# Performance work log

Measured on AMD Instinct MI355X. Metric: run time of the kernel, lower is better.

The kernel has to match this reference:

```python
import jax, jax.numpy as jnp
import numpy as np

DIM = 128
LAYERS = 3
N_NODES = 50000
N_EDGES = 640000
LN_EPS = 1e-5


def setup_inputs() -> dict:
    key = jax.random.key(0)
    ks = jax.random.split(key, 10)
    s = 1.0 / np.sqrt(DIM)
    x = jax.random.normal(ks[0], (N_NODES, DIM), dtype=jnp.float32)
    edge_index = jax.random.randint(ks[1], (2, N_EDGES), 0, N_NODES, dtype=jnp.int64)
    in_w = jax.random.uniform(ks[2], (DIM, DIM), jnp.float32, -s, s)
    in_b = jax.random.uniform(ks[3], (DIM,), jnp.float32, -s, s)
    w1 = jax.random.uniform(ks[4], (LAYERS, DIM, DIM), jnp.float32, -s, s)
    b1 = jax.random.uniform(ks[5], (LAYERS, DIM), jnp.float32, -s, s)
    w2 = jax.random.uniform(ks[6], (LAYERS, DIM, DIM), jnp.float32, -s, s)
    b2 = jax.random.uniform(ks[7], (LAYERS, DIM), jnp.float32, -s, s)
    ln_g = jnp.ones((LAYERS, DIM), jnp.float32)
    ln_b = jnp.zeros((LAYERS, DIM), jnp.float32)
    return {"x": x, "edge_index": edge_index, "in_w": in_w, "in_b": in_b,
            "w1": w1, "b1": b1, "w2": w2, "b2": b2, "ln_g": ln_g, "ln_b": ln_b}


def _layer_norm(z, g, b):
    mu = jnp.mean(z, axis=-1, keepdims=True)
    var = jnp.mean(jnp.square(z - mu), axis=-1, keepdims=True)
    return (z - mu) * jax.lax.rsqrt(var + LN_EPS) * g + b


def reference(x, edge_index, in_w, in_b, w1, b1, w2, b2, ln_g, ln_b):
    src, dst = edge_index[0], edge_index[1]
    n = x.shape[0]
    # degree is identical every layer in the original; compute once (same math)
    deg = jax.ops.segment_sum(jnp.ones(dst.shape, x.dtype), dst, num_segments=n)
    deg = jnp.maximum(deg, 1.0)[:, None]  # [N,1]
    h = x @ in_w + in_b  # [N,D]
    for i in range(w1.shape[0]):
        m = jax.ops.segment_sum(h[src], dst, num_segments=n) / deg  # gather+scatter
        mlp = jax.nn.relu(m @ w1[i] + b1[i]) @ w2[i] + b2[i]
        h = _layer_norm(h + mlp, ln_g[i], ln_b[i])
    return h
```

## Files before the change

### kernel.cpp

```cpp
#include <hip/hip_runtime.h>
#include <hip/hip_fp8.h>

#define DIM 128
#define LN_EPS 1e-5f

typedef __attribute__((ext_vector_type(8))) short s16x8;
typedef __attribute__((ext_vector_type(4))) float f32x4;
typedef __attribute__((ext_vector_type(2))) float f32x2;
typedef __attribute__((ext_vector_type(4))) unsigned int u32x4;
typedef __attribute__((ext_vector_type(2))) unsigned int u32x2;

__device__ __forceinline__ unsigned short f2bf(float f) {
    unsigned u = __float_as_uint(f);
    unsigned r = u + 0x7fffu + ((u >> 16) & 1u);
    return (unsigned short)(r >> 16);
}
__device__ __forceinline__ float bf2f(unsigned short b) {
    return __uint_as_float(((unsigned)b) << 16);
}
__device__ __forceinline__ unsigned char f2fp8(float f) {
    return (unsigned char)__hip_cvt_float_to_fp8(f, __HIP_SATFINITE, __HIP_E4M3);
}
__device__ __forceinline__ void acc_fp8x4(float* a, unsigned v) {
    f32x2 lo = __builtin_amdgcn_cvt_pk_f32_fp8(v, false);
    f32x2 hi = __builtin_amdgcn_cvt_pk_f32_fp8(v, true);
    a[0] += lo[0]; a[1] += lo[1]; a[2] += hi[0]; a[3] += hi[1];
}
__device__ __forceinline__ void acc_fp8x16(float* a, u32x4 v) {
    acc_fp8x4(a + 0,  v[0]);
    acc_fp8x4(a + 4,  v[1]);
    acc_fp8x4(a + 8,  v[2]);
    acc_fp8x4(a + 12, v[3]);
}


__global__ void count_deg(const int* __restrict__ dst, int E, int* __restrict__ counts) {
    int i = (blockIdx.x * 256 + threadIdx.x) * 4;
    if (i + 3 < E) {
        int4 d = *(const int4*)(dst + i);
        atomicAdd(&counts[d.x], 1);
        atomicAdd(&counts[d.y], 1);
        atomicAdd(&counts[d.z], 1);
        atomicAdd(&counts[d.w], 1);
    } else {
        for (int j = i; j < E; ++j) atomicAdd(&counts[dst[j]], 1);
    }
}

__global__ __launch_bounds__(256) void scan_partials(const int* __restrict__ counts, int n,
                                                     int* __restrict__ bsum) {
    int base = blockIdx.x * 1024 + threadIdx.x * 4;
    int s = 0;
#pragma unroll
    for (int j = 0; j < 4; ++j) {
        int i = base + j;
        if (i < n) s += counts[i];
    }
#pragma unroll
    for (int off = 32; off > 0; off >>= 1) s += __shfl_xor(s, off, 64);
    __shared__ int wsum[4];
    int lane = threadIdx.x & 63, wid = threadIdx.x >> 6;
    if (lane == 0) wsum[wid] = s;
    __syncthreads();
    if (threadIdx.x == 0) bsum[blockIdx.x] = wsum[0] + wsum[1] + wsum[2] + wsum[3];
}

__global__ __launch_bounds__(64) void scan_bsums(const int* __restrict__ bsum,
                                                 int* __restrict__ bofs, int nb,
                                                 int* __restrict__ rowptr, int N, int E) {
    int lane = threadIdx.x;
    int carry = 0;
    for (int base = 0; base < nb; base += 64) {
        int v = (base + lane < nb) ? bsum[base + lane] : 0;
        int incl = v;
#pragma unroll
        for (int off = 1; off < 64; off <<= 1) {
            int t = __shfl_up(incl, off, 64);
            if (lane >= off) incl += t;
        }
        if (base + lane < nb) bofs[base + lane] = carry + incl - v;
        carry += __shfl(incl, 63, 64);
    }
    if (lane == 0) rowptr[N] = E;
}

__global__ __launch_bounds__(256) void scan_final(const int* __restrict__ counts, int n,
                                                  const int* __restrict__ bofs,
                                                  int* __restrict__ rowptr,
                                                  int* __restrict__ cursor,
                                                  float* __restrict__ dinv) {
    int base = blockIdx.x * 1024 + threadIdx.x * 4;
    int v[4];
#pragma unroll
    for (int j = 0; j < 4; ++j) {
        int i = base + j;
        v[j] = (i < n) ? counts[i] : 0;
    }
    int tsum = v[0] + v[1] + v[2] + v[3];
    int lane = threadIdx.x & 63, wid = threadIdx.x >> 6;
    int incl = tsum;
#pragma unroll
    for (int off = 1; off < 64; off <<= 1) {
        int t = __shfl_up(incl, off, 64);
        if (lane >= off) incl += t;
    }
    __shared__ int wsum[4];
    if (lane == 63) wsum[wid] = incl;
    __syncthreads();
    int wofs = 0;
    for (int w = 0; w < 4; ++w)
        if (w < wid) wofs += wsum[w];
    int excl = bofs[blockIdx.x] + wofs + (incl - tsum);
#pragma unroll
    for (int j = 0; j < 4; ++j) {
        int i = base + j;
        if (i < n) {
            rowptr[i] = excl;
            cursor[i] = excl;
            dinv[i] = 1.0f / (float)((v[j] > 1) ? v[j] : 1);
            excl += v[j];
        }
    }
}

__global__ void fill_csr(const int* __restrict__ src, const int* __restrict__ dst, int E,
                         int* __restrict__ cursor, int* __restrict__ srcidx) {
    int i = (blockIdx.x * 256 + threadIdx.x) * 4;
    if (i + 3 < E) {
        int4 s = *(const int4*)(src + i);
        int4 d = *(const int4*)(dst + i);
        int p0 = atomicAdd(&cursor[d.x], 1); srcidx[p0] = s.x;
        int p1 = atomicAdd(&cursor[d.y], 1); srcidx[p1] = s.y;
        int p2 = atomicAdd(&cursor[d.z], 1); srcidx[p2] = s.z;
        int p3 = atomicAdd(&cursor[d.w], 1); srcidx[p3] = s.w;
    } else {
        for (int j = i; j < E; ++j) {
            int p = atomicAdd(&cursor[dst[j]], 1);
            srcidx[p] = src[j];
        }
    }
}


__global__ __launch_bounds__(256) void cvt_weights(const float* __restrict__ in_w,
                                                   const float* __restrict__ w1,
                                                   const float* __restrict__ w2,
                                                   unsigned short* __restrict__ wt, int L) {
    int mat = blockIdx.x >> 3, part = blockIdx.x & 7;
    const float* src;
    if (mat == 0) src = in_w;
    else if (mat <= L) src = w1 + (size_t)(mat - 1) * DIM * DIM;
    else src = w2 + (size_t)(mat - 1 - L) * DIM * DIM;
    unsigned short* dst = wt + (size_t)mat * DIM * DIM;
    int base = part * 2048 + threadIdx.x;
#pragma unroll
    for (int j = 0; j < 8; ++j) {
        int i = base + j * 256;
        int k = i >> 7, n = i & 127;
        dst[n * DIM + k] = f2bf(src[i]);
    }
}


__global__ __launch_bounds__(256) void gemm_bias_mfma(const float* __restrict__ x,
                                                      const unsigned short* __restrict__ Wt,
                                                      const float* __restrict__ bias,
                                                      unsigned short* __restrict__ hb,
                                                      unsigned char* __restrict__ h8, int N) {
    int tid = threadIdx.x;
    int s = tid >> 6, lane = tid & 63;
    int quad = lane >> 4, l16 = lane & 15;
    int r0 = blockIdx.x * 16;
    int cs = s * 32;
    int arow = r0 + l16;
    bool av = arow < N;

    f32x4 acc[2];
    acc[0] = (f32x4){0.f, 0.f, 0.f, 0.f};
    acc[1] = (f32x4){0.f, 0.f, 0.f, 0.f};

    const float4* xp = (const float4*)(x + ((size_t)(av ? arow : 0) << 7)) + quad * 2;
#pragma unroll
    for (int k0 = 0; k0 < 128; k0 += 32) {
        s16x8 a = {0, 0, 0, 0, 0, 0, 0, 0};
        if (av) {
            float4 f0 = xp[k0 / 4];
            float4 f1 = xp[k0 / 4 + 1];
            a[0] = (short)f2bf(f0.x); a[1] = (short)f2bf(f0.y);
            a[2] = (short)f2bf(f0.z); a[3] = (short)f2bf(f0.w);
            a[4] = (short)f2bf(f1.x); a[5] = (short)f2bf(f1.y);
            a[6] = (short)f2bf(f1.z); a[7] = (short)f2bf(f1.w);
        }
        s16x8 b0 = *(const s16x8*)(Wt + ((size_t)(cs + l16) << 7) + quad * 8 + k0);
        s16x8 b1 = *(const s16x8*)(Wt + ((size_t)(cs + 16 + l16) << 7) + quad * 8 + k0);
        acc[0] = __builtin_amdgcn_mfma_f32_16x16x32_bf16(a, b0, acc[0], 0, 0, 0);
        acc[1] = __builtin_amdgcn_mfma_f32_16x16x32_bf16(a, b1, acc[1], 0, 0, 0);
    }

#pragma unroll
    for (int c = 0; c < 2; ++c) {
        int col = cs + c * 16 + l16;
        float bv = bias[col];
#pragma unroll
        for (int reg = 0; reg < 4; ++reg) {
            int grow = r0 + quad * 4 + reg;
            if (grow < N) {
                float o = acc[c][reg] + bv;
                hb[((size_t)grow << 7) + col] = f2bf(o);
                h8[((size_t)grow << 7) + col] = f2fp8(o);
            }
        }
    }
}


__global__ __launch_bounds__(256) void aggregate(const unsigned char* __restrict__ h8in,
                                                 const int* __restrict__ rowptr,
                                                 const int* __restrict__ srcidx,
                                                 const float* __restrict__ dinv,
                                                 unsigned short* __restrict__ mout, int N) {
    int tid = threadIdx.x;
    int w = tid >> 6, lane = tid & 63;
    int g = lane >> 3, li = lane & 7;
    int nd = blockIdx.x * 32 + w * 8 + g;
    bool nv = nd < N;

    int e  = nv ? rowptr[nd] : 0;
    int ee = nv ? rowptr[nd + 1] : 0;
    float di = nv ? dinv[nd] : 0.f;

    const unsigned char* hsl = h8in + li * 16;

    float a[16];
#pragma unroll
    for (int j = 0; j < 16; ++j) a[j] = 0.f;

#define GIDX(jj) (((jj) < ee) ? srcidx[(jj)] : -1)
    int jA = e;
    int iA0 = GIDX(jA + 0), iA1 = GIDX(jA + 1), iA2 = GIDX(jA + 2), iA3 = GIDX(jA + 3);
    u32x4 A0 = {0, 0, 0, 0}, A1 = {0, 0, 0, 0}, A2 = {0, 0, 0, 0}, A3 = {0, 0, 0, 0};
    if (iA0 >= 0) A0 = *(const u32x4*)(hsl + ((size_t)iA0 << 7));
    if (iA1 >= 0) A1 = *(const u32x4*)(hsl + ((size_t)iA1 << 7));
    if (iA2 >= 0) A2 = *(const u32x4*)(hsl + ((size_t)iA2 << 7));
    if (iA3 >= 0) A3 = *(const u32x4*)(hsl + ((size_t)iA3 << 7));
    int jB = jA + 4;
    int iB0 = GIDX(jB + 0), iB1 = GIDX(jB + 1), iB2 = GIDX(jB + 2), iB3 = GIDX(jB + 3);

    while (__any(jA < ee)) {
        u32x4 B0 = {0, 0, 0, 0}, B1v = {0, 0, 0, 0}, B2v = {0, 0, 0, 0}, B3 = {0, 0, 0, 0};
        if (iB0 >= 0) B0  = *(const u32x4*)(hsl + ((size_t)iB0 << 7));
        if (iB1 >= 0) B1v = *(const u32x4*)(hsl + ((size_t)iB1 << 7));
        if (iB2 >= 0) B2v = *(const u32x4*)(hsl + ((size_t)iB2 << 7));
        if (iB3 >= 0) B3  = *(const u32x4*)(hsl + ((size_t)iB3 << 7));
        int jC = jB + 4;
        int iC0 = GIDX(jC + 0), iC1 = GIDX(jC + 1), iC2 = GIDX(jC + 2), iC3 = GIDX(jC + 3);
        acc_fp8x16(a, A0);
        acc_fp8x16(a, A1);
        acc_fp8x16(a, A2);
        acc_fp8x16(a, A3);
        jA = jB; A0 = B0; A1 = B1v; A2 = B2v; A3 = B3;
        jB = jC; iB0 = iC0; iB1 = iC1; iB2 = iC2; iB3 = iC3;
    }
#undef GIDX

    if (nv) {
        u32x4 o0, o1;
#pragma unroll
        for (int j = 0; j < 4; ++j) {
            unsigned lo0 = f2bf(a[2 * j]     * di);
            unsigned hi0 = f2bf(a[2 * j + 1] * di);
            o0[j] = lo0 | (hi0 << 16);
            unsigned lo1 = f2bf(a[8 + 2 * j]     * di);
            unsigned hi1 = f2bf(a[8 + 2 * j + 1] * di);
            o1[j] = lo1 | (hi1 << 16);
        }
        unsigned short* mp = mout + ((size_t)nd << 7) + li * 16;
        *(u32x4*)(mp)     = o0;
        *(u32x4*)(mp + 8) = o1;
    }
}


__global__ __launch_bounds__(256) void mlp_ln(const unsigned short* __restrict__ hin,
                                              const unsigned short* __restrict__ m,
                                              const unsigned short* __restrict__ W1t,
                                              const float* __restrict__ B1,
                                              const unsigned short* __restrict__ W2t,
                                              const float* __restrict__ B2,
                                              const float* __restrict__ G,
                                              const float* __restrict__ Bb,
                                              unsigned short* __restrict__ hout,
                                              unsigned char* __restrict__ h8out,
                                              float* __restrict__ out_f32, int N) {
    __shared__ unsigned short M[32][132];
    __shared__ unsigned short P[32][132];
    __shared__ float s1p[4][32], s2p[4][32];

    int tid = threadIdx.x;
    int w = tid >> 6, lane = tid & 63;
    int quad = lane >> 4, l16 = lane & 15;
    int r0 = blockIdx.x * 32;
    int cs = w * 32;

#pragma unroll
    for (int cc = 0; cc < 2; ++cc) {
        int c = tid + cc * 256;
        int row = c >> 4, colc = (c & 15) * 8;
        int grow = r0 + row;
        u32x4 v = {0, 0, 0, 0};
        if (grow < N) v = *(const u32x4*)(m + ((size_t)grow << 7) + colc);
        *(u32x4*)(&M[row][colc]) = v;
    }
    __syncthreads();

    unsigned short hvr[2][2][4];
#pragma unroll
    for (int rt = 0; rt < 2; ++rt) {
#pragma unroll
        for (int c = 0; c < 2; ++c) {
            int col = cs + c * 16 + l16;
#pragma unroll
            for (int reg = 0; reg < 4; ++reg) {
                int grow = r0 + rt * 16 + quad * 4 + reg;
                hvr[rt][c][reg] = (grow < N) ? hin[((size_t)grow << 7) + col] : (unsigned short)0;
            }
        }
    }

    f32x4 ac1[2][2];
    ac1[0][0] = (f32x4){0.f, 0.f, 0.f, 0.f}; ac1[0][1] = (f32x4){0.f, 0.f, 0.f, 0.f};
    ac1[1][0] = (f32x4){0.f, 0.f, 0.f, 0.f}; ac1[1][1] = (f32x4){0.f, 0.f, 0.f, 0.f};
#pragma unroll
    for (int k0 = 0; k0 < 128; k0 += 32) {
        s16x8 b0 = *(const s16x8*)(W1t + ((size_t)(cs + l16) << 7) + quad * 8 + k0);
        s16x8 b1 = *(const s16x8*)(W1t + ((size_t)(cs + 16 + l16) << 7) + quad * 8 + k0);
        s16x8 a0 = *(const s16x8*)(&M[l16][quad * 8 + k0]);
        s16x8 a1 = *(const s16x8*)(&M[16 + l16][quad * 8 + k0]);
        ac1[0][0] = __builtin_amdgcn_mfma_f32_16x16x32_bf16(a0, b0, ac1[0][0], 0, 0, 0);
        ac1[0][1] = __builtin_amdgcn_mfma_f32_16x16x32_bf16(a0, b1, ac1[0][1], 0, 0, 0);
        ac1[1][0] = __builtin_amdgcn_mfma_f32_16x16x32_bf16(a1, b0, ac1[1][0], 0, 0, 0);
        ac1[1][1] = __builtin_amdgcn_mfma_f32_16x16x32_bf16(a1, b1, ac1[1][1], 0, 0, 0);
    }
#pragma unroll
    for (int rt = 0; rt < 2; ++rt) {
#pragma unroll
        for (int c = 0; c < 2; ++c) {
            int col = cs + c * 16 + l16;
            float bv = B1[col];
#pragma unroll
            for (int reg = 0; reg < 4; ++reg) {
                float v = fmaxf(ac1[rt][c][reg] + bv, 0.f);
                P[rt * 16 + quad * 4 + reg][col] = f2bf(v);
            }
        }
    }
    __syncthreads();

    f32x4 ac2[2][2];
    ac2[0][0] = (f32x4){0.f, 0.f, 0.f, 0.f}; ac2[0][1] = (f32x4){0.f, 0.f, 0.f, 0.f};
    ac2[1][0] = (f32x4){0.f, 0.f, 0.f, 0.f}; ac2[1][1] = (f32x4){0.f, 0.f, 0.f, 0.f};
#pragma unroll
    for (int k0 = 0; k0 < 128; k0 += 32) {
        s16x8 b0 = *(const s16x8*)(W2t + ((size_t)(cs + l16) << 7) + quad * 8 + k0);
        s16x8 b1 = *(const s16x8*)(W2t + ((size_t)(cs + 16 + l16) << 7) + quad * 8 + k0);
        s16x8 a0 = *(const s16x8*)(&P[l16][quad * 8 + k0]);
        s16x8 a1 = *(const s16x8*)(&P[16 + l16][quad * 8 + k0]);
        ac2[0][0] = __builtin_amdgcn_mfma_f32_16x16x32_bf16(a0, b0, ac2[0][0], 0, 0, 0);
        ac2[0][1] = __builtin_amdgcn_mfma_f32_16x16x32_bf16(a0, b1, ac2[0][1], 0, 0, 0);
        ac2[1][0] = __builtin_amdgcn_mfma_f32_16x16x32_bf16(a1, b0, ac2[1][0], 0, 0, 0);
        ac2[1][1] = __builtin_amdgcn_mfma_f32_16x16x32_bf16(a1, b1, ac2[1][1], 0, 0, 0);
    }

    float z[2][2][4];
    float ps1[2][4] = {{0, 0, 0, 0}, {0, 0, 0, 0}};
    float ps2[2][4] = {{0, 0, 0, 0}, {0, 0, 0, 0}};
#pragma unroll
    for (int rt = 0; rt < 2; ++rt) {
#pragma unroll
        for (int c = 0; c < 2; ++c) {
            int col = cs + c * 16 + l16;
            float b2v = B2[col];
#pragma unroll
            for (int reg = 0; reg < 4; ++reg) {
                float hv = bf2f(hvr[rt][c][reg]);
                float zz = ac2[rt][c][reg] + b2v + hv;
                z[rt][c][reg] = zz;
                ps1[rt][reg] += zz;
                ps2[rt][reg] += zz * zz;
            }
        }
    }
#pragma unroll
    for (int off = 1; off < 16; off <<= 1) {
#pragma unroll
        for (int rt = 0; rt < 2; ++rt) {
#pragma unroll
            for (int reg = 0; reg < 4; ++reg) {
                ps1[rt][reg] += __shfl_xor(ps1[rt][reg], off, 64);
                ps2[rt][reg] += __shfl_xor(ps2[rt][reg], off, 64);
            }
        }
    }
    if (l16 == 0) {
#pragma unroll
        for (int rt = 0; rt < 2; ++rt) {
#pragma unroll
            for (int reg = 0; reg < 4; ++reg) {
                s1p[w][rt * 16 + quad * 4 + reg] = ps1[rt][reg];
                s2p[w][rt * 16 + quad * 4 + reg] = ps2[rt][reg];
            }
        }
    }
    __syncthreads();

#pragma unroll
    for (int rt = 0; rt < 2; ++rt) {
#pragma unroll
        for (int reg = 0; reg < 4; ++reg) {
            int row = rt * 16 + quad * 4 + reg;
            float S1 = s1p[0][row] + s1p[1][row] + s1p[2][row] + s1p[3][row];
            float S2 = s2p[0][row] + s2p[1][row] + s2p[2][row] + s2p[3][row];
            float mean = S1 * (1.0f / 128.0f);
            float var = S2 * (1.0f / 128.0f) - mean * mean;
            float rs = rsqrtf(var + LN_EPS);
            int grow = r0 + row;
            if (grow < N) {
#pragma unroll
                for (int c = 0; c < 2; ++c) {
                    int col = cs + c * 16 + l16;
                    float o = (z[rt][c][reg] - mean) * rs * G[col] + Bb[col];
                    if (out_f32) {
                        out_f32[((size_t)grow << 7) + col] = o;
                    } else {
                        hout[((size_t)grow << 7) + col] = f2bf(o);
                        h8out[((size_t)grow << 7) + col] = f2fp8(o);
                    }
                }
            }
        }
    }
}


extern "C" void kernel_launch(void* const* d_in, const int* in_sizes, int n_in,
                              void* d_out, int out_size, void* d_ws, size_t ws_size,
                              hipStream_t stream) {
    const float* x    = (const float*)d_in[0];
    const int*   ei   = (const int*)d_in[1];
    const float* in_w = (const float*)d_in[2];
    const float* in_b = (const float*)d_in[3];
    const float* w1   = (const float*)d_in[4];
    const float* b1   = (const float*)d_in[5];
    const float* w2   = (const float*)d_in[6];
    const float* b2   = (const float*)d_in[7];
    const float* ln_g = (const float*)d_in[8];
    const float* ln_b = (const float*)d_in[9];

    const int N = in_sizes[0] / DIM;
    const int E = in_sizes[1] / 2;
    const int LAYERS = in_sizes[4] / (DIM * DIM);

    const int* e_src = ei;
    const int* e_dst = ei + E;

    char* ws = (char*)d_ws;
    unsigned short* hb0    = (unsigned short*)ws;  ws += (size_t)N * DIM * 2;
    unsigned short* hb1    = (unsigned short*)ws;  ws += (size_t)N * DIM * 2;
    unsigned char*  h8a    = (unsigned char*)ws;   ws += (size_t)N * DIM;
    unsigned char*  h8b    = (unsigned char*)ws;   ws += (size_t)N * DIM;
    int*            counts = (int*)ws;             ws += (size_t)N * 4;
    int*            rowptr = (int*)ws;             ws += (size_t)(N + 1) * 4;
    int*            cursor = (int*)ws;             ws += (size_t)N * 4;
    float*          dinv   = (float*)ws;           ws += (size_t)N * 4;
    int*            srcidx = (int*)ws;             ws += (size_t)E * 4;
    int*            bsum   = (int*)ws;             ws += 4096;
    int*            bofs   = (int*)ws;             ws += 4096;
    unsigned short* wt     = (unsigned short*)ws;  ws += (size_t)(2 * LAYERS + 1) * DIM * DIM * 2;
    unsigned short* mbuf   = (unsigned short*)ws;  ws += (size_t)N * DIM * 2;

    const int nScanBlocks = (N + 1023) / 1024;
    const int nMat = 2 * LAYERS + 1;

    (void)hipMemsetAsync(counts, 0, (size_t)N * 4, stream);
    count_deg<<<(E + 1023) / 1024, 256, 0, stream>>>(e_dst, E, counts);
    scan_partials<<<nScanBlocks, 256, 0, stream>>>(counts, N, bsum);
    scan_bsums<<<1, 64, 0, stream>>>(bsum, bofs, nScanBlocks, rowptr, N, E);
    scan_final<<<nScanBlocks, 256, 0, stream>>>(counts, N, bofs, rowptr, cursor, dinv);
    fill_csr<<<(E + 1023) / 1024, 256, 0, stream>>>(e_src, e_dst, E, cursor, srcidx);
    cvt_weights<<<nMat * 8, 256, 0, stream>>>(in_w, w1, w2, wt, LAYERS);

    const unsigned short* in_wt = wt;
    const unsigned short* w1t   = wt + (size_t)DIM * DIM;
    const unsigned short* w2t   = wt + (size_t)(1 + LAYERS) * DIM * DIM;

    gemm_bias_mfma<<<(N + 15) / 16, 256, 0, stream>>>(x, in_wt, in_b, hb0, h8a, N);

    int tile_grid = (N + 31) / 32;
    unsigned short* hin  = hb0;  unsigned char* h8in  = h8a;
    unsigned short* hout = hb1;  unsigned char* h8out = h8b;
    for (int i = 0; i < LAYERS; ++i) {
        float* out = (i == LAYERS - 1) ? (float*)d_out : nullptr;
        aggregate<<<tile_grid, 256, 0, stream>>>(h8in, rowptr, srcidx, dinv, mbuf, N);
        mlp_ln<<<tile_grid, 256, 0, stream>>>(hin, mbuf,
                                              w1t + (size_t)i * DIM * DIM, b1 + (size_t)i * DIM,
                                              w2t + (size_t)i * DIM * DIM, b2 + (size_t)i * DIM,
                                              ln_g + (size_t)i * DIM, ln_b + (size_t)i * DIM,
                                              hout, h8out, out, N);
        unsigned short* t = hin; hin = hout; hout = t;
        unsigned char* t8 = h8in; h8in = h8out; h8out = t8;
    }
}
```

Baseline: 335.4 us.

## Split fp8 feature table into column planes and aggregate each plane separately

The fp8 copy of the node features is stored as two 64-column planes ([2][N][64]), and the aggregation runs twice, once per plane. Each plane is then half the size of the full table, so it is more likely to stay resident in cache during the random neighbour gathers. The setup is also trimmed: the weight conversion and degree counting are fused into one launch, and the single-block offset scan is folded into scan_final, where each block sums the preceding partial sums itself. The cost is twice the index and rowptr traffic and an extra kernel launch per layer.

```diff
diff --git a/kernel.cpp b/kernel.cpp
--- a/kernel.cpp
+++ b/kernel.cpp
@@ -33,17 +33,43 @@
     acc_fp8x4(a + 12, v[3]);
 }
 
-
-__global__ void count_deg(const int* __restrict__ dst, int E, int* __restrict__ counts) {
-    int i = (blockIdx.x * 256 + threadIdx.x) * 4;
-    if (i + 3 < E) {
-        int4 d = *(const int4*)(dst + i);
-        atomicAdd(&counts[d.x], 1);
-        atomicAdd(&counts[d.y], 1);
-        atomicAdd(&counts[d.z], 1);
-        atomicAdd(&counts[d.w], 1);
+__device__ __forceinline__ size_t h8addr(int col, int row, int N) {
+    return (size_t)(col >> 6) * ((size_t)N * 64) + ((size_t)row << 6) + (col & 63);
+}
+
+
+__global__ __launch_bounds__(256) void prep(const float* __restrict__ in_w,
+                                            const float* __restrict__ w1,
+                                            const float* __restrict__ w2,
+                                            unsigned short* __restrict__ wt, int L,
+                                            const int* __restrict__ dst, int E,
+                                            int* __restrict__ counts, int nWblk) {
+    if ((int)blockIdx.x < nWblk) {
+        int mat = blockIdx.x >> 3, part = blockIdx.x & 7;
+        const float* src;
+        if (mat == 0) src = in_w;
+        else if (mat <= L) src = w1 + (size_t)(mat - 1) * DIM * DIM;
+        else src = w2 + (size_t)(mat - 1 - L) * DIM * DIM;
+        unsigned short* dstw = wt + (size_t)mat * DIM * DIM;
+        int base = part * 2048 + threadIdx.x;
+#pragma unroll
+        for (int j = 0; j < 8; ++j) {
+            int i = base + j * 256;
+            int k = i >> 7, n = i & 127;
+            dstw[n * DIM + k] = f2bf(src[i]);
+        }
     } else {
-        for (int j = i; j < E; ++j) atomicAdd(&counts[dst[j]], 1);
+        int b = blockIdx.x - nWblk;
+        int i = (b * 256 + threadIdx.x) * 4;
+        if (i + 3 < E) {
+            int4 d = *(const int4*)(dst + i);
+            atomicAdd(&counts[d.x], 1);
+            atomicAdd(&counts[d.y], 1);
+            atomicAdd(&counts[d.z], 1);
+            atomicAdd(&counts[d.w], 1);
+        } else {
+            for (int j = i; j < E; ++j) atomicAdd(&counts[dst[j]], 1);
+        }
     }
 }
 
@@ -65,31 +91,26 @@
     if (threadIdx.x == 0) bsum[blockIdx.x] = wsum[0] + wsum[1] + wsum[2] + wsum[3];
 }
 
-__global__ __launch_bounds__(64) void scan_bsums(const int* __restrict__ bsum,
-                                                 int* __restrict__ bofs, int nb,
-                                                 int* __restrict__ rowptr, int N, int E) {
-    int lane = threadIdx.x;
-    int carry = 0;
-    for (int base = 0; base < nb; base += 64) {
-        int v = (base + lane < nb) ? bsum[base + lane] : 0;
-        int incl = v;
-#pragma unroll
-        for (int off = 1; off < 64; off <<= 1) {
-            int t = __shfl_up(incl, off, 64);
-            if (lane >= off) incl += t;
-        }
-        if (base + lane < nb) bofs[base + lane] = carry + incl - v;
-        carry += __shfl(incl, 63, 64);
-    }
-    if (lane == 0) rowptr[N] = E;
-}
-
 __global__ __launch_bounds__(256) void scan_final(const int* __restrict__ counts, int n,
-                                                  const int* __restrict__ bofs,
+                                                  const int* __restrict__ bsum, int nScan,
                                                   int* __restrict__ rowptr,
                                                   int* __restrict__ cursor,
-                                                  float* __restrict__ dinv) {
-    int base = blockIdx.x * 1024 + threadIdx.x * 4;
+                                                  float* __restrict__ dinv, int E) {
+    __shared__ int s_bofs;
+    __shared__ int wsum[4];
+    int tid = threadIdx.x;
+    int lane = tid & 63, wid = tid >> 6;
+
+    if (tid < 64) {
+        int acc = 0;
+        for (int i = lane; i < (int)blockIdx.x; i += 64) acc += bsum[i];
+#pragma unroll
+        for (int off = 32; off > 0; off >>= 1) acc += __shfl_xor(acc, off, 64);
+        if (lane == 0) s_bofs = acc;
+    }
+    if (blockIdx.x == 0 && tid == 0) rowptr[n] = E;
+
+    int base = blockIdx.x * 1024 + tid * 4;
     int v[4];
 #pragma unroll
     for (int j = 0; j < 4; ++j) {
@@ -97,20 +118,18 @@
         v[j] = (i < n) ? counts[i] : 0;
     }
     int tsum = v[0] + v[1] + v[2] + v[3];
-    int lane = threadIdx.x & 63, wid = threadIdx.x >> 6;
     int incl = tsum;
 #pragma unroll
     for (int off = 1; off < 64; off <<= 1) {
         int t = __shfl_up(incl, off, 64);
         if (lane >= off) incl += t;
     }
-    __shared__ int wsum[4];
     if (lane == 63) wsum[wid] = incl;
     __syncthreads();
     int wofs = 0;
     for (int w = 0; w < 4; ++w)
         if (w < wid) wofs += wsum[w];
-    int excl = bofs[blockIdx.x] + wofs + (incl - tsum);
+    int excl = s_bofs + wofs + (incl - tsum);
 #pragma unroll
     for (int j = 0; j < 4; ++j) {
         int i = base + j;
@@ -142,26 +161,6 @@
 }
 
 
-__global__ __launch_bounds__(256) void cvt_weights(const float* __restrict__ in_w,
-                                                   const float* __restrict__ w1,
-                                                   const float* __restrict__ w2,
-                                                   unsigned short* __restrict__ wt, int L) {
-    int mat = blockIdx.x >> 3, part = blockIdx.x & 7;
-    const float* src;
-    if (mat == 0) src = in_w;
-    else if (mat <= L) src = w1 + (size_t)(mat - 1) * DIM * DIM;
-    else src = w2 + (size_t)(mat - 1 - L) * DIM * DIM;
-    unsigned short* dst = wt + (size_t)mat * DIM * DIM;
-    int base = part * 2048 + threadIdx.x;
-#pragma unroll
-    for (int j = 0; j < 8; ++j) {
-        int i = base + j * 256;
-        int k = i >> 7, n = i & 127;
-        dst[n * DIM + k] = f2bf(src[i]);
-    }
-}
-
-
 __global__ __launch_bounds__(256) void gemm_bias_mfma(const float* __restrict__ x,
                                                       const unsigned short* __restrict__ Wt,
                                                       const float* __restrict__ bias,
@@ -207,29 +206,30 @@
             if (grow < N) {
                 float o = acc[c][reg] + bv;
                 hb[((size_t)grow << 7) + col] = f2bf(o);
-                h8[((size_t)grow << 7) + col] = f2fp8(o);
-            }
-        }
-    }
-}
-
-
-__global__ __launch_bounds__(256) void aggregate(const unsigned char* __restrict__ h8in,
+                h8[h8addr(col, grow, N)] = f2fp8(o);
+            }
+        }
+    }
+}
+
+
+__global__ __launch_bounds__(256) void aggregate(const unsigned char* __restrict__ h8plane,
                                                  const int* __restrict__ rowptr,
                                                  const int* __restrict__ srcidx,
                                                  const float* __restrict__ dinv,
-                                                 unsigned short* __restrict__ mout, int N) {
+                                                 unsigned short* __restrict__ mout,
+                                                 int N, int plane) {
     int tid = threadIdx.x;
     int w = tid >> 6, lane = tid & 63;
-    int g = lane >> 3, li = lane & 7;
-    int nd = blockIdx.x * 32 + w * 8 + g;
+    int g = lane >> 2, li = lane & 3;
+    int nd = blockIdx.x * 64 + w * 16 + g;
     bool nv = nd < N;
 
     int e  = nv ? rowptr[nd] : 0;
     int ee = nv ? rowptr[nd + 1] : 0;
     float di = nv ? dinv[nd] : 0.f;
 
-    const unsigned char* hsl = h8in + li * 16;
+    const unsigned char* hsl = h8plane + li * 16;
 
     float a[16];
 #pragma unroll
@@ -239,19 +239,19 @@
     int jA = e;
     int iA0 = GIDX(jA + 0), iA1 = GIDX(jA + 1), iA2 = GIDX(jA + 2), iA3 = GIDX(jA + 3);
     u32x4 A0 = {0, 0, 0, 0}, A1 = {0, 0, 0, 0}, A2 = {0, 0, 0, 0}, A3 = {0, 0, 0, 0};
-    if (iA0 >= 0) A0 = *(const u32x4*)(hsl + ((size_t)iA0 << 7));
-    if (iA1 >= 0) A1 = *(const u32x4*)(hsl + ((size_t)iA1 << 7));
-    if (iA2 >= 0) A2 = *(const u32x4*)(hsl + ((size_t)iA2 << 7));
-    if (iA3 >= 0) A3 = *(const u32x4*)(hsl + ((size_t)iA3 << 7));
+    if (iA0 >= 0) A0 = *(const u32x4*)(hsl + ((size_t)iA0 << 6));
+    if (iA1 >= 0) A1 = *(const u32x4*)(hsl + ((size_t)iA1 << 6));
+    if (iA2 >= 0) A2 = *(const u32x4*)(hsl + ((size_t)iA2 << 6));
+    if (iA3 >= 0) A3 = *(const u32x4*)(hsl + ((size_t)iA3 << 6));
     int jB = jA + 4;
     int iB0 = GIDX(jB + 0), iB1 = GIDX(jB + 1), iB2 = GIDX(jB + 2), iB3 = GIDX(jB + 3);
 
     while (__any(jA < ee)) {
         u32x4 B0 = {0, 0, 0, 0}, B1v = {0, 0, 0, 0}, B2v = {0, 0, 0, 0}, B3 = {0, 0, 0, 0};
-        if (iB0 >= 0) B0  = *(const u32x4*)(hsl + ((size_t)iB0 << 7));
-        if (iB1 >= 0) B1v = *(const u32x4*)(hsl + ((size_t)iB1 << 7));
-        if (iB2 >= 0) B2v = *(const u32x4*)(hsl + ((size_t)iB2 << 7));
-        if (iB3 >= 0) B3  = *(const u32x4*)(hsl + ((size_t)iB3 << 7));
+        if (iB0 >= 0) B0  = *(const u32x4*)(hsl + ((size_t)iB0 << 6));
+        if (iB1 >= 0) B1v = *(const u32x4*)(hsl + ((size_t)iB1 << 6));
+        if (iB2 >= 0) B2v = *(const u32x4*)(hsl + ((size_t)iB2 << 6));
+        if (iB3 >= 0) B3  = *(const u32x4*)(hsl + ((size_t)iB3 << 6));
         int jC = jB + 4;
         int iC0 = GIDX(jC + 0), iC1 = GIDX(jC + 1), iC2 = GIDX(jC + 2), iC3 = GIDX(jC + 3);
         acc_fp8x16(a, A0);
@@ -274,7 +274,7 @@
             unsigned hi1 = f2bf(a[8 + 2 * j + 1] * di);
             o1[j] = lo1 | (hi1 << 16);
         }
-        unsigned short* mp = mout + ((size_t)nd << 7) + li * 16;
+        unsigned short* mp = mout + ((size_t)nd << 7) + plane * 64 + li * 16;
         *(u32x4*)(mp)     = o0;
         *(u32x4*)(mp + 8) = o1;
     }
@@ -433,7 +433,7 @@
                         out_f32[((size_t)grow << 7) + col] = o;
                     } else {
                         hout[((size_t)grow << 7) + col] = f2bf(o);
-                        h8out[((size_t)grow << 7) + col] = f2fp8(o);
+                        h8out[h8addr(col, grow, N)] = f2fp8(o);
                     }
                 }
             }
@@ -474,20 +474,20 @@
     float*          dinv   = (float*)ws;           ws += (size_t)N * 4;
     int*            srcidx = (int*)ws;             ws += (size_t)E * 4;
     int*            bsum   = (int*)ws;             ws += 4096;
-    int*            bofs   = (int*)ws;             ws += 4096;
     unsigned short* wt     = (unsigned short*)ws;  ws += (size_t)(2 * LAYERS + 1) * DIM * DIM * 2;
     unsigned short* mbuf   = (unsigned short*)ws;  ws += (size_t)N * DIM * 2;
 
     const int nScanBlocks = (N + 1023) / 1024;
     const int nMat = 2 * LAYERS + 1;
+    const int nWblk = nMat * 8;
 
     (void)hipMemsetAsync(counts, 0, (size_t)N * 4, stream);
-    count_deg<<<(E + 1023) / 1024, 256, 0, stream>>>(e_dst, E, counts);
+    prep<<<nWblk + (E + 1023) / 1024, 256, 0, stream>>>(in_w, w1, w2, wt, LAYERS,
+                                                        e_dst, E, counts, nWblk);
     scan_partials<<<nScanBlocks, 256, 0, stream>>>(counts, N, bsum);
-    scan_bsums<<<1, 64, 0, stream>>>(bsum, bofs, nScanBlocks, rowptr, N, E);
-    scan_final<<<nScanBlocks, 256, 0, stream>>>(counts, N, bofs, rowptr, cursor, dinv);
+    scan_final<<<nScanBlocks, 256, 0, stream>>>(counts, N, bsum, nScanBlocks,
+                                                rowptr, cursor, dinv, E);
     fill_csr<<<(E + 1023) / 1024, 256, 0, stream>>>(e_src, e_dst, E, cursor, srcidx);
-    cvt_weights<<<nMat * 8, 256, 0, stream>>>(in_w, w1, w2, wt, LAYERS);
 
     const unsigned short* in_wt = wt;
     const unsigned short* w1t   = wt + (size_t)DIM * DIM;
@@ -495,17 +495,20 @@
 
     gemm_bias_mfma<<<(N + 15) / 16, 256, 0, stream>>>(x, in_wt, in_b, hb0, h8a, N);
 
-    int tile_grid = (N + 31) / 32;
+    int agg_grid = (N + 63) / 64;
+    int mlp_grid = (N + 31) / 32;
     unsigned short* hin  = hb0;  unsigned char* h8in  = h8a;
     unsigned short* hout = hb1;  unsigned char* h8out = h8b;
     for (int i = 0; i < LAYERS; ++i) {
         float* out = (i == LAYERS - 1) ? (float*)d_out : nullptr;
-        aggregate<<<tile_grid, 256, 0, stream>>>(h8in, rowptr, srcidx, dinv, mbuf, N);
-        mlp_ln<<<tile_grid, 256, 0, stream>>>(hin, mbuf,
-                                              w1t + (size_t)i * DIM * DIM, b1 + (size_t)i * DIM,
-                                              w2t + (size_t)i * DIM * DIM, b2 + (size_t)i * DIM,
-                                              ln_g + (size_t)i * DIM, ln_b + (size_t)i * DIM,
-                                              hout, h8out, out, N);
+        aggregate<<<agg_grid, 256, 0, stream>>>(h8in, rowptr, srcidx, dinv, mbuf, N, 0);
+        aggregate<<<agg_grid, 256, 0, stream>>>(h8in + (size_t)N * 64, rowptr, srcidx, dinv,
+                                                mbuf, N, 1);
+        mlp_ln<<<mlp_grid, 256, 0, stream>>>(hin, mbuf,
+                                             w1t + (size_t)i * DIM * DIM, b1 + (size_t)i * DIM,
+                                             w2t + (size_t)i * DIM * DIM, b2 + (size_t)i * DIM,
+                                             ln_g + (size_t)i * DIM, ln_b + (size_t)i * DIM,
+                                             hout, h8out, out, N);
         unsigned short* t = hin; hin = hout; hout = t;
         unsigned char* t8 = h8in; h8in = h8out; h8out = t8;
     }
```

Result: slower. 362.2 us (+8.0%).

## Merge graph-prep kernels: fuse degree count, single-pass scan, CSR fill with projection

Applied to the files above, without the earlier changes.

Weight conversion and degree counting now run as one launch, with the block index picking the role. The three-kernel prefix scan becomes a single kernel in which each block redundantly sums all counts before its own range. CSR filling is merged with the input projection GEMM so the two independent jobs share one launch. The goal is fewer launches and serial gaps in the setup phase, at the cost of redundant prefix reads in the scan and mixed workloads sharing a grid.

```diff
diff --git a/kernel.cpp b/kernel.cpp
--- a/kernel.cpp
+++ b/kernel.cpp
@@ -8,7 +8,6 @@
 typedef __attribute__((ext_vector_type(4))) float f32x4;
 typedef __attribute__((ext_vector_type(2))) float f32x2;
 typedef __attribute__((ext_vector_type(4))) unsigned int u32x4;
-typedef __attribute__((ext_vector_type(2))) unsigned int u32x2;
 
 __device__ __forceinline__ unsigned short f2bf(float f) {
     unsigned u = __float_as_uint(f);
@@ -34,62 +33,66 @@
 }
 
 
-__global__ void count_deg(const int* __restrict__ dst, int E, int* __restrict__ counts) {
-    int i = (blockIdx.x * 256 + threadIdx.x) * 4;
-    if (i + 3 < E) {
-        int4 d = *(const int4*)(dst + i);
-        atomicAdd(&counts[d.x], 1);
-        atomicAdd(&counts[d.y], 1);
-        atomicAdd(&counts[d.z], 1);
-        atomicAdd(&counts[d.w], 1);
+__global__ __launch_bounds__(256) void prep(const float* __restrict__ in_w,
+                                            const float* __restrict__ w1,
+                                            const float* __restrict__ w2,
+                                            unsigned short* __restrict__ wt, int L,
+                                            const int* __restrict__ dst, int E,
+                                            int* __restrict__ counts, int nWblk) {
+    if ((int)blockIdx.x < nWblk) {
+        int mat = blockIdx.x >> 3, part = blockIdx.x & 7;
+        const float* src;
+        if (mat == 0) src = in_w;
+        else if (mat <= L) src = w1 + (size_t)(mat - 1) * DIM * DIM;
+        else src = w2 + (size_t)(mat - 1 - L) * DIM * DIM;
+        unsigned short* dstw = wt + (size_t)mat * DIM * DIM;
+        int base = part * 2048 + threadIdx.x;
+#pragma unroll
+        for (int j = 0; j < 8; ++j) {
+            int i = base + j * 256;
+            int k = i >> 7, n = i & 127;
+            dstw[n * DIM + k] = f2bf(src[i]);
+        }
     } else {
-        for (int j = i; j < E; ++j) atomicAdd(&counts[dst[j]], 1);
-    }
-}
-
-__global__ __launch_bounds__(256) void scan_partials(const int* __restrict__ counts, int n,
-                                                     int* __restrict__ bsum) {
-    int base = blockIdx.x * 1024 + threadIdx.x * 4;
-    int s = 0;
-#pragma unroll
-    for (int j = 0; j < 4; ++j) {
-        int i = base + j;
-        if (i < n) s += counts[i];
-    }
-#pragma unroll
-    for (int off = 32; off > 0; off >>= 1) s += __shfl_xor(s, off, 64);
+        int b = blockIdx.x - nWblk;
+        int i = (b * 256 + threadIdx.x) * 4;
+        if (i + 3 < E) {
+            int4 d = *(const int4*)(dst + i);
+            atomicAdd(&counts[d.x], 1);
+            atomicAdd(&counts[d.y], 1);
+            atomicAdd(&counts[d.z], 1);
+            atomicAdd(&counts[d.w], 1);
+        } else {
+            for (int j = i; j < E; ++j) atomicAdd(&counts[dst[j]], 1);
+        }
+    }
+}
+
+
+__global__ __launch_bounds__(256) void scan_all(const int* __restrict__ counts, int n,
+                                                int* __restrict__ rowptr,
+                                                int* __restrict__ cursor,
+                                                float* __restrict__ dinv, int E) {
     __shared__ int wsum[4];
-    int lane = threadIdx.x & 63, wid = threadIdx.x >> 6;
-    if (lane == 0) wsum[wid] = s;
-    __syncthreads();
-    if (threadIdx.x == 0) bsum[blockIdx.x] = wsum[0] + wsum[1] + wsum[2] + wsum[3];
-}
-
-__global__ __launch_bounds__(64) void scan_bsums(const int* __restrict__ bsum,
-                                                 int* __restrict__ bofs, int nb,
-                                                 int* __restrict__ rowptr, int N, int E) {
-    int lane = threadIdx.x;
-    int carry = 0;
-    for (int base = 0; base < nb; base += 64) {
-        int v = (base + lane < nb) ? bsum[base + lane] : 0;
-        int incl = v;
-#pragma unroll
-        for (int off = 1; off < 64; off <<= 1) {
-            int t = __shfl_up(incl, off, 64);
-            if (lane >= off) incl += t;
-        }
-        if (base + lane < nb) bofs[base + lane] = carry + incl - v;
-        carry += __shfl(incl, 63, 64);
-    }
-    if (lane == 0) rowptr[N] = E;
-}
-
-__global__ __launch_bounds__(256) void scan_final(const int* __restrict__ counts, int n,
-                                                  const int* __restrict__ bofs,
-                                                  int* __restrict__ rowptr,
-                                                  int* __restrict__ cursor,
-                                                  float* __restrict__ dinv) {
-    int base = blockIdx.x * 1024 + threadIdx.x * 4;
+    int tid = threadIdx.x;
+    int lane = tid & 63, wid = tid >> 6;
+
+    int limit = blockIdx.x * 1024;
+    int acc = 0;
+    for (int i = tid * 4; i < limit; i += 1024) {
+        int4 c4 = *(const int4*)(counts + i);
+        acc += c4.x + c4.y + c4.z + c4.w;
+    }
+#pragma unroll
+    for (int off = 32; off > 0; off >>= 1) acc += __shfl_xor(acc, off, 64);
+    if (lane == 0) wsum[wid] = acc;
+    __syncthreads();
+    int bofs = wsum[0] + wsum[1] + wsum[2] + wsum[3];
+    __syncthreads();
+
+    if (blockIdx.x == 0 && tid == 0) rowptr[n] = E;
+
+    int base = blockIdx.x * 1024 + tid * 4;
     int v[4];
 #pragma unroll
     for (int j = 0; j < 4; ++j) {
@@ -97,20 +100,18 @@
         v[j] = (i < n) ? counts[i] : 0;
     }
     int tsum = v[0] + v[1] + v[2] + v[3];
-    int lane = threadIdx.x & 63, wid = threadIdx.x >> 6;
     int incl = tsum;
 #pragma unroll
     for (int off = 1; off < 64; off <<= 1) {
         int t = __shfl_up(incl, off, 64);
         if (lane >= off) incl += t;
     }
-    __shared__ int wsum[4];
     if (lane == 63) wsum[wid] = incl;
     __syncthreads();
     int wofs = 0;
     for (int w = 0; w < 4; ++w)
         if (w < wid) wofs += wsum[w];
-    int excl = bofs[blockIdx.x] + wofs + (incl - tsum);
+    int excl = bofs + wofs + (incl - tsum);
 #pragma unroll
     for (int j = 0; j < 4; ++j) {
         int i = base + j;
@@ -123,91 +124,74 @@
     }
 }
 
-__global__ void fill_csr(const int* __restrict__ src, const int* __restrict__ dst, int E,
-                         int* __restrict__ cursor, int* __restrict__ srcidx) {
-    int i = (blockIdx.x * 256 + threadIdx.x) * 4;
-    if (i + 3 < E) {
-        int4 s = *(const int4*)(src + i);
-        int4 d = *(const int4*)(dst + i);
-        int p0 = atomicAdd(&cursor[d.x], 1); srcidx[p0] = s.x;
-        int p1 = atomicAdd(&cursor[d.y], 1); srcidx[p1] = s.y;
-        int p2 = atomicAdd(&cursor[d.z], 1); srcidx[p2] = s.z;
-        int p3 = atomicAdd(&cursor[d.w], 1); srcidx[p3] = s.w;
+
+__global__ __launch_bounds__(256) void fill_proj(const float* __restrict__ x,
+                                                 const unsigned short* __restrict__ Wt,
+                                                 const float* __restrict__ bias,
+                                                 unsigned short* __restrict__ hb,
+                                                 unsigned char* __restrict__ h8, int N,
+                                                 const int* __restrict__ src,
+                                                 const int* __restrict__ dst, int E,
+                                                 int* __restrict__ cursor,
+                                                 int* __restrict__ srcidx, int gemmBlocks) {
+    int tid = threadIdx.x;
+    if ((int)blockIdx.x < gemmBlocks) {
+        int s = tid >> 6, lane = tid & 63;
+        int quad = lane >> 4, l16 = lane & 15;
+        int r0 = blockIdx.x * 16;
+        int cs = s * 32;
+        int arow = r0 + l16;
+        bool av = arow < N;
+
+        f32x4 acc0 = (f32x4){0.f, 0.f, 0.f, 0.f};
+        f32x4 acc1 = (f32x4){0.f, 0.f, 0.f, 0.f};
+
+        const float4* xp = (const float4*)(x + ((size_t)(av ? arow : 0) << 7)) + quad * 2;
+#pragma unroll
+        for (int k0 = 0; k0 < 128; k0 += 32) {
+            s16x8 a = {0, 0, 0, 0, 0, 0, 0, 0};
+            if (av) {
+                float4 f0 = xp[k0 / 4];
+                float4 f1 = xp[k0 / 4 + 1];
+                a[0] = (short)f2bf(f0.x); a[1] = (short)f2bf(f0.y);
+                a[2] = (short)f2bf(f0.z); a[3] = (short)f2bf(f0.w);
+                a[4] = (short)f2bf(f1.x); a[5] = (short)f2bf(f1.y);
+                a[6] = (short)f2bf(f1.z); a[7] = (short)f2bf(f1.w);
+            }
+            s16x8 b0 = *(const s16x8*)(Wt + ((size_t)(cs + l16) << 7) + quad * 8 + k0);
+            s16x8 b1 = *(const s16x8*)(Wt + ((size_t)(cs + 16 + l16) << 7) + quad * 8 + k0);
+            acc0 = __builtin_amdgcn_mfma_f32_16x16x32_bf16(a, b0, acc0, 0, 0, 0);
+            acc1 = __builtin_amdgcn_mfma_f32_16x16x32_bf16(a, b1, acc1, 0, 0, 0);
+        }
+
+#pragma unroll
+        for (int c = 0; c < 2; ++c) {
+            int col = cs + c * 16 + l16;
+            float bv = bias[col];
+#pragma unroll
+            for (int reg = 0; reg < 4; ++reg) {
+                int grow = r0 + quad * 4 + reg;
+                if (grow < N) {
+                    float o = (c == 0 ? acc0[reg] : acc1[reg]) + bv;
+                    hb[((size_t)grow << 7) + col] = f2bf(o);
+                    h8[((size_t)grow << 7) + col] = f2fp8(o);
+                }
+            }
+        }
     } else {
-        for (int j = i; j < E; ++j) {
-            int p = atomicAdd(&cursor[dst[j]], 1);
-            srcidx[p] = src[j];
-        }
-    }
-}
-
-
-__global__ __launch_bounds__(256) void cvt_weights(const float* __restrict__ in_w,
-                                                   const float* __restrict__ w1,
-                                                   const float* __restrict__ w2,
-                                                   unsigned short* __restrict__ wt, int L) {
-    int mat = blockIdx.x >> 3, part = blockIdx.x & 7;
-    const float* src;
-    if (mat == 0) src = in_w;
-    else if (mat <= L) src = w1 + (size_t)(mat - 1) * DIM * DIM;
-    else src = w2 + (size_t)(mat - 1 - L) * DIM * DIM;
-    unsigned short* dst = wt + (size_t)mat * DIM * DIM;
-    int base = part * 2048 + threadIdx.x;
-#pragma unroll
-    for (int j = 0; j < 8; ++j) {
-        int i = base + j * 256;
-        int k = i >> 7, n = i & 127;
-        dst[n * DIM + k] = f2bf(src[i]);
-    }
-}
-
-
-__global__ __launch_bounds__(256) void gemm_bias_mfma(const float* __restrict__ x,
-                                                      const unsigned short* __restrict__ Wt,
-                                                      const float* __restrict__ bias,
-                                                      unsigned short* __restrict__ hb,
-                                                      unsigned char* __restrict__ h8, int N) {
-    int tid = threadIdx.x;
-    int s = tid >> 6, lane = tid & 63;
-    int quad = lane >> 4, l16 = lane & 15;
-    int r0 = blockIdx.x * 16;
-    int cs = s * 32;
-    int arow = r0 + l16;
-    bool av = arow < N;
-
-    f32x4 acc[2];
-    acc[0] = (f32x4){0.f, 0.f, 0.f, 0.f};
-    acc[1] = (f32x4){0.f, 0.f, 0.f, 0.f};
-
-    const float4* xp = (const float4*)(x + ((size_t)(av ? arow : 0) << 7)) + quad * 2;
-#pragma unroll
-    for (int k0 = 0; k0 < 128; k0 += 32) {
-        s16x8 a = {0, 0, 0, 0, 0, 0, 0, 0};
-        if (av) {
-            float4 f0 = xp[k0 / 4];
-            float4 f1 = xp[k0 / 4 + 1];
-            a[0] = (short)f2bf(f0.x); a[1] = (short)f2bf(f0.y);
-            a[2] = (short)f2bf(f0.z); a[3] = (short)f2bf(f0.w);
-            a[4] = (short)f2bf(f1.x); a[5] = (short)f2bf(f1.y);
-            a[6] = (short)f2bf(f1.z); a[7] = (short)f2bf(f1.w);
-        }
-        s16x8 b0 = *(const s16x8*)(Wt + ((size_t)(cs + l16) << 7) + quad * 8 + k0);
-        s16x8 b1 = *(const s16x8*)(Wt + ((size_t)(cs + 16 + l16) << 7) + quad * 8 + k0);
-        acc[0] = __builtin_amdgcn_mfma_f32_16x16x32_bf16(a, b0, acc[0], 0, 0, 0);
-        acc[1] = __builtin_amdgcn_mfma_f32_16x16x32_bf16(a, b1, acc[1], 0, 0, 0);
-    }
-
-#pragma unroll
-    for (int c = 0; c < 2; ++c) {
-        int col = cs + c * 16 + l16;
-        float bv = bias[col];
-#pragma unroll
-        for (int reg = 0; reg < 4; ++reg) {
-            int grow = r0 + quad * 4 + reg;
-            if (grow < N) {
-                float o = acc[c][reg] + bv;
-                hb[((size_t)grow << 7) + col] = f2bf(o);
-                h8[((size_t)grow << 7) + col] = f2fp8(o);
+        int b = blockIdx.x - gemmBlocks;
+        int i = (b * 256 + tid) * 4;
+        if (i + 3 < E) {
+            int4 s4 = *(const int4*)(src + i);
+            int4 d4 = *(const int4*)(dst + i);
+            int p0 = atomicAdd(&cursor[d4.x], 1); srcidx[p0] = s4.x;
+            int p1 = atomicAdd(&cursor[d4.y], 1); srcidx[p1] = s4.y;
+            int p2 = atomicAdd(&cursor[d4.z], 1); srcidx[p2] = s4.z;
+            int p3 = atomicAdd(&cursor[d4.w], 1); srcidx[p3] = s4.w;
+        } else {
+            for (int j = i; j < E; ++j) {
+                int p = atomicAdd(&cursor[dst[j]], 1);
+                srcidx[p] = src[j];
             }
         }
     }
@@ -473,27 +457,25 @@
     int*            cursor = (int*)ws;             ws += (size_t)N * 4;
     float*          dinv   = (float*)ws;           ws += (size_t)N * 4;
     int*            srcidx = (int*)ws;             ws += (size_t)E * 4;
-    int*            bsum   = (int*)ws;             ws += 4096;
-    int*            bofs   = (int*)ws;             ws += 4096;
     unsigned short* wt     = (unsigned short*)ws;  ws += (size_t)(2 * LAYERS + 1) * DIM * DIM * 2;
     unsigned short* mbuf   = (unsigned short*)ws;  ws += (size_t)N * DIM * 2;
 
     const int nScanBlocks = (N + 1023) / 1024;
     const int nMat = 2 * LAYERS + 1;
+    const int nWblk = nMat * 8;
+    const int gemmBlocks = (N + 15) / 16;
+    const int fillBlocks = (E + 1023) / 1024;
 
     (void)hipMemsetAsync(counts, 0, (size_t)N * 4, stream);
-    count_deg<<<(E + 1023) / 1024, 256, 0, stream>>>(e_dst, E, counts);
-    scan_partials<<<nScanBlocks, 256, 0, stream>>>(counts, N, bsum);
-    scan_bsums<<<1, 64, 0, stream>>>(bsum, bofs, nScanBlocks, rowptr, N, E);
-    scan_final<<<nScanBlocks, 256, 0, stream>>>(counts, N, bofs, rowptr, cursor, dinv);
-    fill_csr<<<(E + 1023) / 1024, 256, 0, stream>>>(e_src, e_dst, E, cursor, srcidx);
-    cvt_weights<<<nMat * 8, 256, 0, stream>>>(in_w, w1, w2, wt, LAYERS);
-
-    const unsigned short* in_wt = wt;
-    const unsigned short* w1t   = wt + (size_t)DIM * DIM;
-    const unsigned short* w2t   = wt + (size_t)(1 + LAYERS) * DIM * DIM;
-
-    gemm_bias_mfma<<<(N + 15) / 16, 256, 0, stream>>>(x, in_wt, in_b, hb0, h8a, N);
+    prep<<<nWblk + (E + 1023) / 1024, 256, 0, stream>>>(in_w, w1, w2, wt, LAYERS,
+                                                        e_dst, E, counts, nWblk);
+    scan_all<<<nScanBlocks, 256, 0, stream>>>(counts, N, rowptr, cursor, dinv, E);
+    fill_proj<<<gemmBlocks + fillBlocks, 256, 0, stream>>>(x, wt, in_b, hb0, h8a, N,
+                                                           e_src, e_dst, E, cursor, srcidx,
+                                                           gemmBlocks);
+
+    const unsigned short* w1t = wt + (size_t)DIM * DIM;
+    const unsigned short* w2t = wt + (size_t)(1 + LAYERS) * DIM * DIM;
 
     int tile_grid = (N + 31) / 32;
     unsigned short* hin  = hb0;  unsigned char* h8in  = h8a;
```

Result: no change. 330.3 us (-1.5%).
